# Optimization experiments

Hardware: AMD Instinct MI355X
Metric: run time of the kernel (lower is better)

The kernel has to match this reference:

```python
import jax, jax.numpy as jnp
import numpy as np

HEAD = 8
D_Q = 64
NEG_INF = -1e9
EPS = 1e-9


def setup_inputs() -> dict:
    key = jax.random.key(0)
    ks = jax.random.split(key, 5)
    bs, seq_len, d_model = 4, 1024, 512
    context = jax.random.normal(ks[0], (bs, seq_len, d_model), dtype=jnp.float32)
    attention_mask = jnp.ones((bs, seq_len), dtype=jnp.int32)
    # nn.Linear default init: U(-1/sqrt(fan_in), 1/sqrt(fan_in))
    bound = 1.0 / np.sqrt(d_model)
    Wq = jax.random.uniform(ks[1], (HEAD * D_Q, d_model), jnp.float32, -bound, bound)
    bq = jax.random.uniform(ks[2], (HEAD * D_Q,), jnp.float32, -bound, bound)
    Wk = jax.random.uniform(ks[3], (HEAD * D_Q, d_model), jnp.float32, -bound, bound)
    bk = jax.random.uniform(ks[4], (HEAD * D_Q,), jnp.float32, -bound, bound)
    return {"context": context, "attention_mask": attention_mask,
            "Wq": Wq, "bq": bq, "Wk": Wk, "bk": bk}


def reference(context, attention_mask, Wq, bq, Wk, bk):
    bs, seq_len, d_model = context.shape
    # structural masks
    after_mask = jnp.eye(seq_len, k=1, dtype=jnp.int32)    # superdiagonal
    prev_mask = jnp.eye(seq_len, k=-1, dtype=jnp.int32)    # subdiagonal
    self_mask = jnp.eye(seq_len, dtype=jnp.int32)          # diagonal
    summing_op = jnp.triu(jnp.ones((seq_len, seq_len), jnp.float32))  # upper-tri ones

    # attention_mask & (after + prev): (bs,1,1,S) & (S,S) -> (bs,1,S,S)
    mask = attention_mask[:, None, None, :] & (after_mask + prev_mask)

    # projections -> (bs, head, seq, d_q)
    q = (context @ Wq.T + bq).reshape(bs, seq_len, HEAD, D_Q).transpose(0, 2, 1, 3)
    k = (context @ Wk.T + bk).reshape(bs, seq_len, HEAD, D_Q).transpose(0, 2, 1, 3)

    scores = jnp.einsum('bhqd,bhkd->bhqk', q, k) / d_model
    scores = jnp.where(mask == 0, NEG_INF, scores)
    scores = jax.nn.softmax(scores, axis=-1)

    # geometric-mean fusion of forward/backward neighbor scores
    phrasal_attn = jnp.sqrt(scores * jnp.swapaxes(scores, -2, -1) + EPS)
    # prior_attn = 0 (default): phrasal_attn = 0 + (1-0)*phrasal_attn

    # log-cumsum via triangular matmuls
    p = jnp.where(after_mask == 0, 0.0, jnp.log(phrasal_attn + EPS))  # (bs,h,S,S)
    p = jnp.einsum('bhij,jk->bhik', p, summing_op)
    attn = jnp.exp(jnp.einsum('ij,bhjk->bhik', summing_op, p))
    # zero out on-and-below diagonal (keep strict upper triangle)
    strict_upper = summing_op.astype(jnp.int32) - self_mask
    attn = jnp.where(strict_upper == 0, 0.0, attn)
    attn = attn + jnp.swapaxes(attn, -2, -1) + jnp.where(self_mask == 0, EPS, phrasal_attn)
    return (attn, phrasal_attn)
```

## Files before the change

### kernel.cpp

```cpp
#include <hip/hip_runtime.h>
#include <hip/hip_bf16.h>

#define BS 4
#define SEQ 1024
#define DM 512
#define EPS 1e-9f
#define SQRTEPS 3.16227766e-5f

typedef __attribute__((ext_vector_type(8))) short short8;
typedef __attribute__((ext_vector_type(4))) float floatx4;

__device__ __forceinline__ unsigned short f2bf(float x) {
    unsigned int u = __float_as_uint(x);
    return (unsigned short)((u + 0x7fffu + ((u >> 16) & 1u)) >> 16);
}

__device__ __forceinline__ void bgwrite(float* base, int n_iters, int tid, int nthr) {
    floatx4 v4 = {SQRTEPS, SQRTEPS, SQRTEPS, SQRTEPS};
    for (int j = 0; j < n_iters; ++j)
        *(floatx4*)(base + (size_t)(j * nthr + tid) * 4) = v4;
}

__global__ __launch_bounds__(256) void convert_kernel(
    const float* __restrict__ ctx, const float* __restrict__ Wq,
    const float* __restrict__ Wk, unsigned short* __restrict__ Xbf,
    unsigned short* __restrict__ Wbf, float* __restrict__ phrasal)
{
    const int blk = blockIdx.x, tid = threadIdx.x;
    if (blk >= 256) {
        bgwrite(phrasal + (size_t)(blk - 256) * 8192, 8, tid, 256);
        return;
    }
    int gthr = blk * 256 + tid;
    #pragma unroll
    for (int j = 0; j < 10; ++j) {
        int e4 = gthr + 65536 * j;
        int e  = e4 * 4;
        floatx4 s;
        if (e < 2097152) {
            s = *(const floatx4*)(ctx + e);
        } else {
            int e2 = e - 2097152;
            s = (e2 < 262144) ? *(const floatx4*)(Wq + e2)
                              : *(const floatx4*)(Wk + e2 - 262144);
        }
        ushort2 lo = {f2bf(s.x), f2bf(s.y)}, hi = {f2bf(s.z), f2bf(s.w)};
        unsigned short* dst = (e < 2097152) ? (Xbf + e) : (Wbf + e - 2097152);
        *(ushort2*)dst = lo;
        *(ushort2*)(dst + 2) = hi;
    }
}

#define NGEMM 512
#define LDW 72
#define LDQ 65

__global__ __launch_bounds__(256) void gemmdot_kernel(
    const unsigned short* __restrict__ Xbf, const unsigned short* __restrict__ Wbf,
    const float* __restrict__ bq, const float* __restrict__ bk,
    float* __restrict__ uA, float* __restrict__ vA,
    float* __restrict__ qF, float* __restrict__ kF,
    float* __restrict__ qL, float* __restrict__ kL,
    float* __restrict__ phrasal)
{
    __shared__ char smem[2 * 64 * LDQ * 4];
    unsigned short* Xs  = (unsigned short*)smem;
    unsigned short* Wqs = Xs + 64 * LDW;
    unsigned short* Wks = Wqs + 64 * LDW;
    float* qS = (float*)smem;
    float* kS = qS + 64 * LDQ;

    const int blk = blockIdx.x, tid = threadIdx.x;
    if (blk >= NGEMM) {
        bgwrite(phrasal + (size_t)(768 + blk - NGEMM) * 8192, 8, tid, 256);
        return;
    }

    const int rt = blk >> 3, h = blk & 7;
    const int wv = tid >> 6, lane = tid & 63;
    const int lr = lane & 15, kg = lane >> 4;

    const int r0 = tid >> 3, kc0 = (tid & 7) << 3;
    const unsigned short* Xb  = Xbf + (size_t)(rt * 64) * DM;
    const unsigned short* Wqb = Wbf + (size_t)(h * 64) * DM;
    const unsigned short* Wkb = Wbf + 262144 + (size_t)(h * 64) * DM;

    floatx4 acc_q[4] = {}, acc_k[4] = {};

    for (int k0 = 0; k0 < DM; k0 += 64) {
        uint4 x0  = *(const uint4*)(Xb  + (size_t)r0 * DM + k0 + kc0);
        uint4 x1  = *(const uint4*)(Xb  + (size_t)(r0 + 32) * DM + k0 + kc0);
        uint4 wq0 = *(const uint4*)(Wqb + (size_t)r0 * DM + k0 + kc0);
        uint4 wq1 = *(const uint4*)(Wqb + (size_t)(r0 + 32) * DM + k0 + kc0);
        uint4 wk0 = *(const uint4*)(Wkb + (size_t)r0 * DM + k0 + kc0);
        uint4 wk1 = *(const uint4*)(Wkb + (size_t)(r0 + 32) * DM + k0 + kc0);
        __syncthreads();
        *(uint4*)(Xs  + r0 * LDW + kc0)        = x0;
        *(uint4*)(Xs  + (r0 + 32) * LDW + kc0) = x1;
        *(uint4*)(Wqs + r0 * LDW + kc0)        = wq0;
        *(uint4*)(Wqs + (r0 + 32) * LDW + kc0) = wq1;
        *(uint4*)(Wks + r0 * LDW + kc0)        = wk0;
        *(uint4*)(Wks + (r0 + 32) * LDW + kc0) = wk1;
        __syncthreads();
        #pragma unroll
        for (int ks = 0; ks < 2; ++ks) {
            short8 a = *(const short8*)(Xs + (wv * 16 + lr) * LDW + ks * 32 + kg * 8);
            #pragma unroll
            for (int ni = 0; ni < 4; ++ni) {
                short8 bqf = *(const short8*)(Wqs + (ni * 16 + lr) * LDW + ks * 32 + kg * 8);
                acc_q[ni] = __builtin_amdgcn_mfma_f32_16x16x32_bf16(a, bqf, acc_q[ni], 0, 0, 0);
                short8 bkf = *(const short8*)(Wks + (ni * 16 + lr) * LDW + ks * 32 + kg * 8);
                acc_k[ni] = __builtin_amdgcn_mfma_f32_16x16x32_bf16(a, bkf, acc_k[ni], 0, 0, 0);
            }
        }
    }

    __syncthreads();
    #pragma unroll
    for (int ni = 0; ni < 4; ++ni) {
        float bqv = bq[h * 64 + ni * 16 + lr];
        float bkv = bk[h * 64 + ni * 16 + lr];
        #pragma unroll
        for (int r = 0; r < 4; ++r) {
            int row = wv * 16 + kg * 4 + r;
            qS[row * LDQ + ni * 16 + lr] = acc_q[ni][r] + bqv;
            kS[row * LDQ + ni * 16 + lr] = acc_k[ni][r] + bkv;
        }
    }
    __syncthreads();

    const int eb = (rt * 8 + h) * 64;
    if (tid < 64) {
        qF[eb + tid] = qS[tid];
        kF[eb + tid] = kS[tid];
    } else if (tid >= 192) {
        int l = tid - 192;
        qL[eb + l] = qS[63 * LDQ + l];
        kL[eb + l] = kS[63 * LDQ + l];
    }

    for (int p = wv; p < 63; p += 4) {
        float pu = qS[p * LDQ + lane] * kS[(p + 1) * LDQ + lane];
        float pv = qS[(p + 1) * LDQ + lane] * kS[p * LDQ + lane];
        #pragma unroll
        for (int m = 1; m < 64; m <<= 1) {
            pu += __shfl_xor(pu, m);
            pv += __shfl_xor(pv, m);
        }
        if (lane == 0) {
            int r = rt * 64 + p;
            int idx = (((r >> 10) * 8 + h) << 10) | (r & 1023);
            uA[idx] = pu * (1.0f / DM);
            vA[idx] = pv * (1.0f / DM);
        }
    }
}

__global__ __launch_bounds__(1024) void gscan_kernel(
    const float* __restrict__ uA, const float* __restrict__ vA,
    const float* __restrict__ qF, const float* __restrict__ kF,
    const float* __restrict__ qL, const float* __restrict__ kL,
    const int* __restrict__ am, float* __restrict__ gA, float* __restrict__ CA,
    float* __restrict__ phrasal)
{
    __shared__ float uS[SEQ], vS[SEQ];
    __shared__ float uFix[16], vFix[16];
    __shared__ double wsum[16];

    const int blk = blockIdx.x, i = threadIdx.x;
    if (blk >= 32) {
        bgwrite(phrasal + (size_t)(2816 + blk - 32) * 8192, 2, i, 1024);
        return;
    }

    const int bh = blk, b = bh >> 3, h = bh & 7;
    const int base = bh * SEQ;
    const int wv = i >> 6, lane = i & 63;

    uS[i] = uA[base + i];
    vS[i] = vA[base + i];

    if (wv < 15) {
        int e0 = ((b * 16 + wv) * 8 + h) * 64;
        int e1 = e0 + 8 * 64;
        float pu = qL[e0 + lane] * kF[e1 + lane];
        float pv = qF[e1 + lane] * kL[e0 + lane];
        #pragma unroll
        for (int m = 1; m < 64; m <<= 1) {
            pu += __shfl_xor(pu, m);
            pv += __shfl_xor(pv, m);
        }
        if (lane == 0) { uFix[wv] = pu * (1.0f / DM); vFix[wv] = pv * (1.0f / DM); }
    }
    __syncthreads();
    if ((i & 63) == 63) {
        int j = i >> 6;
        uS[i] = (j < 15) ? uFix[j] : 0.f;
        vS[i] = (j < 15) ? vFix[j] : 0.f;
    }
    __syncthreads();

    float g = 0.f;
    if (i < SEQ - 1) {
        float u = uS[i], vv = vS[i];
        float vm1 = (i > 0) ? vS[i - 1] : 0.f;
        float up1 = uS[i + 1];
        const int* amb = am + b * SEQ;
        int mL = (i > 0) ? amb[i - 1] : 0;
        int mR = amb[i + 1];
        float s_up = mR ? (mL ? 1.f / (1.f + expf(vm1 - u)) : 1.f) : 0.f;
        int mL2 = amb[i];
        int mR2 = (i + 2 < SEQ) ? amb[i + 2] : 0;
        float s_dn = mL2 ? (mR2 ? 1.f / (1.f + expf(up1 - vv)) : 1.f) : 0.f;
        g = sqrtf(s_up * s_dn + EPS);
        gA[base + i] = g;
    }

    double L = (i < SEQ - 1) ? (double)logf(g + EPS) : 0.0;
    double x = L;
    #pragma unroll
    for (int off = 1; off < 64; off <<= 1) {
        double t = __shfl_up(x, off);
        if (lane >= off) x += t;
    }
    if (lane == 63) wsum[wv] = x;
    __syncthreads();
    double pref = 0.0;
    for (int w = 0; w < wv; ++w) pref += wsum[w];
    CA[base + i] = (float)(pref + x - L);
}

__global__ __launch_bounds__(256) void fill_attn(
    const float* __restrict__ gA, const float* __restrict__ CA,
    float* __restrict__ attn, float* __restrict__ phrasal)
{
    const int row = blockIdx.x;
    const int bh  = row >> 10;
    const int i   = row & 1023;
    const int t   = threadIdx.x;

    const float Ci = CA[row];
    floatx4 c4 = *(const floatx4*)(CA + bh * SEQ + t * 4);
    floatx4 av;
    #pragma unroll
    for (int j = 0; j < 4; ++j) {
        int k = t * 4 + j;
        float d = (k > i) ? (c4[j] - Ci) : (Ci - c4[j]);
        av[j] = (k == i) ? SQRTEPS : (__expf(d) + EPS);
    }
    *(floatx4*)(attn + (size_t)row * SEQ + t * 4) = av;

    if (t == 0 && i > 0)
        phrasal[(size_t)row * SEQ + i - 1] = gA[bh * SEQ + i - 1];
    if (t == 1 && i < SEQ - 1)
        phrasal[(size_t)row * SEQ + i + 1] = gA[bh * SEQ + i];
}

extern "C" void kernel_launch(void* const* d_in, const int* in_sizes, int n_in,
                              void* d_out, int out_size, void* d_ws, size_t ws_size,
                              hipStream_t stream) {
    const float* ctx = (const float*)d_in[0];
    const int*   am  = (const int*)d_in[1];
    const float* Wq  = (const float*)d_in[2];
    const float* bq  = (const float*)d_in[3];
    const float* Wk  = (const float*)d_in[4];
    const float* bk  = (const float*)d_in[5];
    float* out = (float*)d_out;

    char* ws = (char*)d_ws;
    unsigned short* Xbf = (unsigned short*)(ws);
    unsigned short* Wbf = (unsigned short*)(ws + 4194304);
    float*          uA  = (float*)(ws + 5242880);
    float*          vA  = (float*)(ws + 5373952);
    float*          gA  = (float*)(ws + 5505024);
    float*          CA  = (float*)(ws + 5636096);
    float*          qF  = (float*)(ws + 5767168);
    float*          kF  = (float*)(ws + 5898240);
    float*          qL  = (float*)(ws + 6029312);
    float*          kL  = (float*)(ws + 6160384);

    float* attn_out    = out;
    float* phrasal_out = out + (size_t)BS * 8 * SEQ * SEQ;

    convert_kernel<<<dim3(256 + 768), 256, 0, stream>>>(ctx, Wq, Wk, Xbf, Wbf, phrasal_out);
    gemmdot_kernel<<<dim3(NGEMM + 2048), 256, 0, stream>>>(
        Xbf, Wbf, bq, bk, uA, vA, qF, kF, qL, kL, phrasal_out);
    gscan_kernel<<<dim3(32 + 1280), 1024, 0, stream>>>(
        uA, vA, qF, kF, qL, kL, am, gA, CA, phrasal_out);
    fill_attn<<<dim3(BS * 8 * SEQ), 256, 0, stream>>>(gA, CA, attn_out, phrasal_out);
}
```

Baseline: 293.2 us.

## Fuse phrasal background fill into the attn fill kernel with nontemporal stores

Removes the background SQRTEPS writes of the phrasal output that were spread across extra blocks of the convert, gemm and scan kernels. A single fill_outputs kernel now writes each attn row together with the matching phrasal row, including its two off-diagonal values, and covers 16 rows per block. Stores use nontemporal hints. The intent is to shorten the earlier kernels and write both large outputs in one streaming pass, at the cost of losing any overlap the background writes had with the compute kernels.

```diff
diff --git a/kernel.cpp b/kernel.cpp
--- a/kernel.cpp
+++ b/kernel.cpp
@@ -15,22 +15,12 @@
     return (unsigned short)((u + 0x7fffu + ((u >> 16) & 1u)) >> 16);
 }
 
-__device__ __forceinline__ void bgwrite(float* base, int n_iters, int tid, int nthr) {
-    floatx4 v4 = {SQRTEPS, SQRTEPS, SQRTEPS, SQRTEPS};
-    for (int j = 0; j < n_iters; ++j)
-        *(floatx4*)(base + (size_t)(j * nthr + tid) * 4) = v4;
-}
-
 __global__ __launch_bounds__(256) void convert_kernel(
     const float* __restrict__ ctx, const float* __restrict__ Wq,
     const float* __restrict__ Wk, unsigned short* __restrict__ Xbf,
-    unsigned short* __restrict__ Wbf, float* __restrict__ phrasal)
+    unsigned short* __restrict__ Wbf)
 {
     const int blk = blockIdx.x, tid = threadIdx.x;
-    if (blk >= 256) {
-        bgwrite(phrasal + (size_t)(blk - 256) * 8192, 8, tid, 256);
-        return;
-    }
     int gthr = blk * 256 + tid;
     #pragma unroll
     for (int j = 0; j < 10; ++j) {
@@ -60,8 +50,7 @@
     const float* __restrict__ bq, const float* __restrict__ bk,
     float* __restrict__ uA, float* __restrict__ vA,
     float* __restrict__ qF, float* __restrict__ kF,
-    float* __restrict__ qL, float* __restrict__ kL,
-    float* __restrict__ phrasal)
+    float* __restrict__ qL, float* __restrict__ kL)
 {
     __shared__ char smem[2 * 64 * LDQ * 4];
     unsigned short* Xs  = (unsigned short*)smem;
@@ -71,10 +60,6 @@
     float* kS = qS + 64 * LDQ;
 
     const int blk = blockIdx.x, tid = threadIdx.x;
-    if (blk >= NGEMM) {
-        bgwrite(phrasal + (size_t)(768 + blk - NGEMM) * 8192, 8, tid, 256);
-        return;
-    }
 
     const int rt = blk >> 3, h = blk & 7;
     const int wv = tid >> 6, lane = tid & 63;
@@ -160,18 +145,13 @@
     const float* __restrict__ uA, const float* __restrict__ vA,
     const float* __restrict__ qF, const float* __restrict__ kF,
     const float* __restrict__ qL, const float* __restrict__ kL,
-    const int* __restrict__ am, float* __restrict__ gA, float* __restrict__ CA,
-    float* __restrict__ phrasal)
+    const int* __restrict__ am, float* __restrict__ gA, float* __restrict__ CA)
 {
     __shared__ float uS[SEQ], vS[SEQ];
     __shared__ float uFix[16], vFix[16];
     __shared__ double wsum[16];
 
     const int blk = blockIdx.x, i = threadIdx.x;
-    if (blk >= 32) {
-        bgwrite(phrasal + (size_t)(2816 + blk - 32) * 8192, 2, i, 1024);
-        return;
-    }
 
     const int bh = blk, b = bh >> 3, h = bh & 7;
     const int base = bh * SEQ;
@@ -230,30 +210,39 @@
     CA[base + i] = (float)(pref + x - L);
 }
 
-__global__ __launch_bounds__(256) void fill_attn(
+#define RPB 16
+
+__global__ __launch_bounds__(256) void fill_outputs(
     const float* __restrict__ gA, const float* __restrict__ CA,
     float* __restrict__ attn, float* __restrict__ phrasal)
 {
-    const int row = blockIdx.x;
-    const int bh  = row >> 10;
-    const int i   = row & 1023;
+    const int blk = blockIdx.x;
     const int t   = threadIdx.x;
-
-    const float Ci = CA[row];
-    floatx4 c4 = *(const floatx4*)(CA + bh * SEQ + t * 4);
-    floatx4 av;
-    #pragma unroll
-    for (int j = 0; j < 4; ++j) {
-        int k = t * 4 + j;
-        float d = (k > i) ? (c4[j] - Ci) : (Ci - c4[j]);
-        av[j] = (k == i) ? SQRTEPS : (__expf(d) + EPS);
-    }
-    *(floatx4*)(attn + (size_t)row * SEQ + t * 4) = av;
-
-    if (t == 0 && i > 0)
-        phrasal[(size_t)row * SEQ + i - 1] = gA[bh * SEQ + i - 1];
-    if (t == 1 && i < SEQ - 1)
-        phrasal[(size_t)row * SEQ + i + 1] = gA[bh * SEQ + i];
+    const int bh  = blk >> 6;
+    const int i0  = (blk & 63) * RPB;
+    const int base = bh * SEQ;
+    const int k0 = t * 4;
+
+    floatx4 c4 = *(const floatx4*)(CA + base + k0);
+
+    for (int r = 0; r < RPB; ++r) {
+        const int i = i0 + r;
+        const size_t row = ((size_t)bh << 10) | (unsigned)i;
+        const float Ci = CA[base + i];
+        const float gm = (i > 0)       ? gA[base + i - 1] : 0.f;
+        const float gp = (i < SEQ - 1) ? gA[base + i]     : 0.f;
+
+        floatx4 av, pv;
+        #pragma unroll
+        for (int j = 0; j < 4; ++j) {
+            int k = k0 + j;
+            float d = (k > i) ? (c4[j] - Ci) : (Ci - c4[j]);
+            av[j] = (k == i) ? SQRTEPS : (__expf(d) + EPS);
+            pv[j] = (k == i - 1) ? gm : ((k == i + 1) ? gp : SQRTEPS);
+        }
+        __builtin_nontemporal_store(av, (floatx4*)(attn    + (row << 10) + k0));
+        __builtin_nontemporal_store(pv, (floatx4*)(phrasal + (row << 10) + k0));
+    }
 }
 
 extern "C" void kernel_launch(void* const* d_in, const int* in_sizes, int n_in,
@@ -282,10 +271,10 @@
     float* attn_out    = out;
     float* phrasal_out = out + (size_t)BS * 8 * SEQ * SEQ;
 
-    convert_kernel<<<dim3(256 + 768), 256, 0, stream>>>(ctx, Wq, Wk, Xbf, Wbf, phrasal_out);
-    gemmdot_kernel<<<dim3(NGEMM + 2048), 256, 0, stream>>>(
-        Xbf, Wbf, bq, bk, uA, vA, qF, kF, qL, kL, phrasal_out);
-    gscan_kernel<<<dim3(32 + 1280), 1024, 0, stream>>>(
-        uA, vA, qF, kF, qL, kL, am, gA, CA, phrasal_out);
-    fill_attn<<<dim3(BS * 8 * SEQ), 256, 0, stream>>>(gA, CA, attn_out, phrasal_out);
-}
+    convert_kernel<<<dim3(256), 256, 0, stream>>>(ctx, Wq, Wk, Xbf, Wbf);
+    gemmdot_kernel<<<dim3(NGEMM), 256, 0, stream>>>(
+        Xbf, Wbf, bq, bk, uA, vA, qF, kF, qL, kL);
+    gscan_kernel<<<dim3(32), 1024, 0, stream>>>(
+        uA, vA, qF, kF, qL, kL, am, gA, CA);
+    fill_outputs<<<dim3(2048), 256, 0, stream>>>(gA, CA, attn_out, phrasal_out);
+}
```

New measurement: 315.2 us. 1.07x slower.
